# Optimization experiments

Hardware: AMD Instinct MI355X
Metric: run time of the kernel (lower is better)

The kernel has to match this reference:

```python
import jax, jax.numpy as jnp
import numpy as np


def setup_inputs() -> dict:
    key = jax.random.key(0)
    k1, k2, k3 = jax.random.split(key, 3)
    B, C, H, W = 64, 512, 32, 32
    l = jax.random.normal(k1, (B, C, H, W), dtype=jnp.float32)
    g = jax.random.normal(k2, (B, C), dtype=jnp.float32)
    # 1x1 Conv2d(C -> 1, bias=False) weight, flattened from [1, C, 1, 1] to [C]
    w = jax.random.normal(k3, (C,), dtype=jnp.float32) * (1.0 / np.sqrt(C))
    return {"l": l, "g": g, "w": w}


def reference(l, g, w):
    B, C, H, W = l.shape
    # broadcast add of global vector, then 1x1 conv == channel dot-product
    x = l + g[:, :, None, None]                      # [B, C, H, W]
    c = jnp.einsum('bchw,c->bhw', x, w)              # [B, H, W]
    # softmax over the flattened spatial dims
    a = jax.nn.softmax(c.reshape(B, -1), axis=1).reshape(B, 1, H, W)
    # attention-weighted spatial pooling of l -> [B, C]
    g_out = jnp.einsum('bchw,bzhw->bc', l, a)
    return (c[:, None, :, :], g_out)
```

## Files before the change

kernel.cpp:

```cpp
#include <hip/hip_runtime.h>

#define B_    64
#define C_    512
#define HW_   1024
#define S_    32
#define NSLAB (HW_ / S_)
#define TPB   512
#define NGRP  (TPB / S_)
#define CPG   (C_ / NGRP)
#define TSTR  (S_ + 1)

__global__ __launch_bounds__(TPB) void k1_slab(
        const float* __restrict__ l,
        const float* __restrict__ g,
        const float* __restrict__ w,
        float* __restrict__ c_out,
        float* __restrict__ U,
        float2* __restrict__ stats) {
    __shared__ float tile[C_ * TSTR];
    __shared__ float e_lds[S_];
    __shared__ float red[S_ * (NGRP + 1)];
    __shared__ float red2[TPB / 64];

    const int blk  = blockIdx.x;
    const int b    = blk >> 5;
    const int slab = blk & (NSLAB - 1);
    const int t    = threadIdx.x;
    const int lane = t & 63;
    const int wid  = t >> 6;

    float p = g[b * C_ + t] * w[t];
    #pragma unroll
    for (int off = 32; off > 0; off >>= 1) p += __shfl_xor(p, off);
    if (lane == 0) red2[wid] = p;

    const float4* l4 = reinterpret_cast<const float4*>(l);
    float4 v[8];
    #pragma unroll
    for (int i = 0; i < 8; ++i) {
        const int k  = i * TPB + t;
        const int ch = k >> 3, j = k & 7;
        v[i] = l4[((size_t)b * C_ + ch) * (HW_ / 4) + slab * (S_ / 4) + j];
    }
    #pragma unroll
    for (int i = 0; i < 8; ++i) {
        const int k  = i * TPB + t;
        const int ch = k >> 3, j = k & 7;
        float* dst = &tile[ch * TSTR + 4 * j];
        dst[0] = v[i].x; dst[1] = v[i].y; dst[2] = v[i].z; dst[3] = v[i].w;
    }
    __syncthreads();

    const int hw  = t & (S_ - 1);
    const int grp = t >> 5;
    float acc = 0.f;
    #pragma unroll 8
    for (int i = 0; i < CPG; ++i) {
        const int ch = grp * CPG + i;
        acc = fmaf(tile[ch * TSTR + hw], w[ch], acc);
    }
    red[hw * (NGRP + 1) + grp] = acc;
    __syncthreads();

    if (t < S_) {
        float c = 0.f;
        #pragma unroll
        for (int gp = 0; gp < NGRP; ++gp) c += red[t * (NGRP + 1) + gp];
        float gw = 0.f;
        #pragma unroll
        for (int i = 0; i < TPB / 64; ++i) gw += red2[i];
        c += gw;
        c_out[(size_t)b * HW_ + slab * S_ + t] = c;

        float m = c;
        #pragma unroll
        for (int off = 16; off > 0; off >>= 1) m = fmaxf(m, __shfl_xor(m, off));
        const float e = __expf(c - m);
        float E = e;
        #pragma unroll
        for (int off = 16; off > 0; off >>= 1) E += __shfl_xor(E, off);
        e_lds[t] = e;
        if (t == 0) stats[b * NSLAB + slab] = make_float2(m, E);
    }
    __syncthreads();

    float ua = 0.f;
    #pragma unroll 8
    for (int h = 0; h < S_; ++h)
        ua = fmaf(tile[t * TSTR + h], e_lds[h], ua);
    U[((size_t)b * NSLAB + slab) * C_ + t] = ua;
}

__global__ __launch_bounds__(256) void k2_finish(
        const float* __restrict__ U,
        const float2* __restrict__ stats,
        float* __restrict__ gout) {
    __shared__ float scale_lds[NSLAB];
    __shared__ float invZ_lds;
    const int b = blockIdx.x;
    const int t = threadIdx.x;

    if (t < NSLAB) {
        const float2 me = stats[b * NSLAB + t];
        float m = me.x;
        #pragma unroll
        for (int off = 16; off > 0; off >>= 1) m = fmaxf(m, __shfl_xor(m, off));
        const float sc = __expf(me.x - m);
        float Z = me.y * sc;
        #pragma unroll
        for (int off = 16; off > 0; off >>= 1) Z += __shfl_xor(Z, off);
        scale_lds[t] = sc;
        if (t == 0) invZ_lds = __frcp_rn(Z);
    }
    __syncthreads();
    const float invZ = invZ_lds;

    #pragma unroll
    for (int cc = 0; cc < C_ / 256; ++cc) {
        const int ch = cc * 256 + t;
        float acc = 0.f;
        #pragma unroll 8
        for (int s = 0; s < NSLAB; ++s)
            acc = fmaf(U[((size_t)b * NSLAB + s) * C_ + ch], scale_lds[s], acc);
        gout[(size_t)b * C_ + ch] = acc * invZ;
    }
}

extern "C" void kernel_launch(void* const* d_in, const int* in_sizes, int n_in,
                              void* d_out, int out_size, void* d_ws, size_t ws_size,
                              hipStream_t stream) {
    const float* l = (const float*)d_in[0];
    const float* g = (const float*)d_in[1];
    const float* w = (const float*)d_in[2];
    float*  c_out = (float*)d_out;
    float*  gout  = (float*)d_out + (size_t)B_ * HW_;
    float*  U     = (float*)d_ws;
    float2* stats = (float2*)(U + (size_t)B_ * NSLAB * C_);

    k1_slab<<<B_ * NSLAB, TPB, 0, stream>>>(l, g, w, c_out, U, stats);
    k2_finish<<<B_, 256, 0, stream>>>(U, stats, gout);
}
```

Measured before the change: 202.7 us.

## Keep slab in registers with shuffle reductions; split finish kernel across channel groups

The slab kernel no longer stages the 64KB l tile in LDS. Each thread keeps its eight float4s in registers, computes partial channel dot products, and reduces them with cross-lane shuffles and a small LDS buffer. The pooled U values are likewise computed from registers with shuffle reductions. This removes the large LDS footprint, which should raise occupancy and cut LDS traffic, at the cost of more shuffles and extra register pressure. The finish kernel now launches 8 blocks per batch, each covering a 64-channel group with a split over slabs, to expose more parallelism.

```diff
diff --git a/kernel.cpp b/kernel.cpp
--- a/kernel.cpp
+++ b/kernel.cpp
@@ -6,9 +6,6 @@
 #define S_    32
 #define NSLAB (HW_ / S_)
 #define TPB   512
-#define NGRP  (TPB / S_)
-#define CPG   (C_ / NGRP)
-#define TSTR  (S_ + 1)
 
 __global__ __launch_bounds__(TPB) void k1_slab(
         const float* __restrict__ l,
@@ -17,10 +14,10 @@
         float* __restrict__ c_out,
         float* __restrict__ U,
         float2* __restrict__ stats) {
-    __shared__ float tile[C_ * TSTR];
+    __shared__ float w_lds[C_];
+    __shared__ float redc[8 * 8 * 4];
+    __shared__ float redg[8];
     __shared__ float e_lds[S_];
-    __shared__ float red[S_ * (NGRP + 1)];
-    __shared__ float red2[TPB / 64];
 
     const int blk  = blockIdx.x;
     const int b    = blk >> 5;
@@ -28,47 +25,50 @@
     const int t    = threadIdx.x;
     const int lane = t & 63;
     const int wid  = t >> 6;
-
-    float p = g[b * C_ + t] * w[t];
-    #pragma unroll
-    for (int off = 32; off > 0; off >>= 1) p += __shfl_xor(p, off);
-    if (lane == 0) red2[wid] = p;
+    const int j    = t & 7;
+    const int co   = t >> 3;
 
     const float4* l4 = reinterpret_cast<const float4*>(l);
     float4 v[8];
     #pragma unroll
+    for (int i = 0; i < 8; ++i)
+        v[i] = l4[((size_t)b * C_ + (i * 64 + co)) * (HW_ / 4)
+                  + slab * (S_ / 4) + j];
+
+    w_lds[t] = w[t];
+    float p = g[b * C_ + t] * w[t];
+    #pragma unroll
+    for (int off = 32; off > 0; off >>= 1) p += __shfl_xor(p, off);
+    if (lane == 0) redg[wid] = p;
+    __syncthreads();
+
+    float4 cp = {0.f, 0.f, 0.f, 0.f};
+    #pragma unroll
     for (int i = 0; i < 8; ++i) {
-        const int k  = i * TPB + t;
-        const int ch = k >> 3, j = k & 7;
-        v[i] = l4[((size_t)b * C_ + ch) * (HW_ / 4) + slab * (S_ / 4) + j];
+        const float wv = w_lds[i * 64 + co];
+        cp.x = fmaf(v[i].x, wv, cp.x);
+        cp.y = fmaf(v[i].y, wv, cp.y);
+        cp.z = fmaf(v[i].z, wv, cp.z);
+        cp.w = fmaf(v[i].w, wv, cp.w);
     }
     #pragma unroll
-    for (int i = 0; i < 8; ++i) {
-        const int k  = i * TPB + t;
-        const int ch = k >> 3, j = k & 7;
-        float* dst = &tile[ch * TSTR + 4 * j];
-        dst[0] = v[i].x; dst[1] = v[i].y; dst[2] = v[i].z; dst[3] = v[i].w;
+    for (int m = 8; m <= 32; m <<= 1) {
+        cp.x += __shfl_xor(cp.x, m);
+        cp.y += __shfl_xor(cp.y, m);
+        cp.z += __shfl_xor(cp.z, m);
+        cp.w += __shfl_xor(cp.w, m);
     }
-    __syncthreads();
-
-    const int hw  = t & (S_ - 1);
-    const int grp = t >> 5;
-    float acc = 0.f;
-    #pragma unroll 8
-    for (int i = 0; i < CPG; ++i) {
-        const int ch = grp * CPG + i;
-        acc = fmaf(tile[ch * TSTR + hw], w[ch], acc);
-    }
-    red[hw * (NGRP + 1) + grp] = acc;
+    if (lane < 8)
+        reinterpret_cast<float4*>(redc)[wid * 8 + lane] = cp;
     __syncthreads();
 
     if (t < S_) {
         float c = 0.f;
         #pragma unroll
-        for (int gp = 0; gp < NGRP; ++gp) c += red[t * (NGRP + 1) + gp];
+        for (int wv = 0; wv < 8; ++wv) c += redc[wv * 32 + t];
         float gw = 0.f;
         #pragma unroll
-        for (int i = 0; i < TPB / 64; ++i) gw += red2[i];
+        for (int i = 0; i < 8; ++i) gw += redg[i];
         c += gw;
         c_out[(size_t)b * HW_ + slab * S_ + t] = c;
 
@@ -84,11 +84,21 @@
     }
     __syncthreads();
 
-    float ua = 0.f;
-    #pragma unroll 8
-    for (int h = 0; h < S_; ++h)
-        ua = fmaf(tile[t * TSTR + h], e_lds[h], ua);
-    U[((size_t)b * NSLAB + slab) * C_ + t] = ua;
+    const float4 e4 = reinterpret_cast<const float4*>(e_lds)[j];
+    float u[8];
+    #pragma unroll
+    for (int i = 0; i < 8; ++i)
+        u[i] = v[i].x * e4.x + v[i].y * e4.y + v[i].z * e4.z + v[i].w * e4.w;
+    #pragma unroll
+    for (int i = 0; i < 8; ++i) {
+        u[i] += __shfl_xor(u[i], 1);
+        u[i] += __shfl_xor(u[i], 2);
+        u[i] += __shfl_xor(u[i], 4);
+    }
+    float uval = u[0];
+    #pragma unroll
+    for (int i = 1; i < 8; ++i) if (j == i) uval = u[i];
+    U[((size_t)b * NSLAB + slab) * C_ + (j * 64 + co)] = uval;
 }
 
 __global__ __launch_bounds__(256) void k2_finish(
@@ -97,8 +107,14 @@
         float* __restrict__ gout) {
     __shared__ float scale_lds[NSLAB];
     __shared__ float invZ_lds;
-    const int b = blockIdx.x;
-    const int t = threadIdx.x;
+    __shared__ float part2[4 * 64];
+
+    const int blk = blockIdx.x;
+    const int b   = blk >> 3;
+    const int cg  = blk & 7;
+    const int t   = threadIdx.x;
+    const int wid = t >> 6;
+    const int cl  = t & 63;
 
     if (t < NSLAB) {
         const float2 me = stats[b * NSLAB + t];
@@ -113,16 +129,20 @@
         if (t == 0) invZ_lds = __frcp_rn(Z);
     }
     __syncthreads();
-    const float invZ = invZ_lds;
 
+    const int ch = cg * 64 + cl;
+    float acc = 0.f;
     #pragma unroll
-    for (int cc = 0; cc < C_ / 256; ++cc) {
-        const int ch = cc * 256 + t;
-        float acc = 0.f;
-        #pragma unroll 8
-        for (int s = 0; s < NSLAB; ++s)
-            acc = fmaf(U[((size_t)b * NSLAB + s) * C_ + ch], scale_lds[s], acc);
-        gout[(size_t)b * C_ + ch] = acc * invZ;
+    for (int si = 0; si < 8; ++si) {
+        const int s = wid * 8 + si;
+        acc = fmaf(U[((size_t)b * NSLAB + s) * C_ + ch], scale_lds[s], acc);
+    }
+    part2[wid * 64 + cl] = acc;
+    __syncthreads();
+
+    if (wid == 0) {
+        float r = part2[cl] + part2[64 + cl] + part2[128 + cl] + part2[192 + cl];
+        gout[(size_t)b * C_ + ch] = r * invZ_lds;
     }
 }
 
@@ -138,5 +158,5 @@
     float2* stats = (float2*)(U + (size_t)B_ * NSLAB * C_);
 
     k1_slab<<<B_ * NSLAB, TPB, 0, stream>>>(l, g, w, c_out, U, stats);
-    k2_finish<<<B_, 256, 0, stream>>>(U, stats, gout);
+    k2_finish<<<B_ * 8, 256, 0, stream>>>(U, stats, gout);
 }
```

Result: faster. 197.6 us (-2.5%).
